# Performance work log

Hardware: AMD Instinct MI355X
Metric: run time of the kernel (lower is better)

The kernel has to match this reference:

```python
import jax, jax.numpy as jnp
import numpy as np

B = 8192
D = 64      # core_size = size ** (1/nr_cores), size = 4096, nr_cores = 2
R = 4       # TT rank
SIZE = D * D


def setup_inputs() -> dict:
    key = jax.random.key(0)
    k_x, k_c0, k_c1, k_b = jax.random.split(key, 4)
    core_std = (2.0 / D) ** 0.5  # kaiming_normal on (-1, d, d) blocks
    x = jax.random.normal(k_x, (B, SIZE), dtype=jnp.float32)
    core0 = core_std * jax.random.normal(k_c0, (D, D, D, R, 1), dtype=jnp.float32)
    core1 = core_std * jax.random.normal(k_c1, (D, D, D, 1, R), dtype=jnp.float32)
    bound = (6.0 / SIZE) ** 0.5  # kaiming_uniform on (1, out_dim)
    bias = jax.random.uniform(k_b, (SIZE,), dtype=jnp.float32, minval=-bound, maxval=bound)
    return {"x": x, "core0": core0, "core1": core1, "bias": bias}


def reference(x, core0, core1, bias):
    # BTT.forward with nr_cores=2, d=D, rank=R
    b = x.shape[0]
    # idx=0: t=1 -> j=D, i=1 ; z: (B, j=D, x=D, i=1, a=1), core: (j=D, x=D, y=D, i=1, b=R, a=1)
    z = x.reshape(b, D, D, 1, 1)
    c0 = core0.reshape(D, D, D, 1, R, 1)
    z = jnp.einsum('Bjxia,jxyiba->Bjyib', z, c0)  # (B, D, D, 1, R)
    # idx=1: t=0 -> j=1, i=D ; z: (B, 1, D, D, R), core: (1, D, D, D, 1, R)
    z = z.reshape(b, 1, D, D, R)
    c1 = core1.reshape(1, D, D, D, 1, R)
    z = jnp.einsum('Bjxia,jxyiba->Bjyib', z, c1)  # (B, 1, D, D, 1)
    return z.reshape(b, -1) + bias
```

## Files before the change

### kernel.cpp

```cpp
#include <hip/hip_runtime.h>


typedef unsigned short ushort_t;
typedef __attribute__((ext_vector_type(8))) short sfrag8;
typedef __attribute__((ext_vector_type(4))) float f32x4;

__device__ inline ushort_t f2bf(float f) {
    unsigned int u = __builtin_bit_cast(unsigned int, f);
    u += 0x7fffu + ((u >> 16) & 1u);
    return (ushort_t)(u >> 16);
}

__global__ __launch_bounds__(256) void prep_c0t(const float* __restrict__ c0,
                                                ushort_t* __restrict__ c0t) {
    __shared__ float tile[64][65];
    const int t = threadIdx.x;
    const int ub = blockIdx.x * 64;
    const int cb = blockIdx.y * 64;
#pragma unroll
    for (int it = 0; it < 16; ++it) {
        const int r = it * 4 + (t >> 6);
        const int c = t & 63;
        tile[r][c] = c0[(size_t)(ub + r) * 256 + cb + c];
    }
    __syncthreads();
#pragma unroll
    for (int it = 0; it < 16; ++it) {
        const int r = it * 4 + (t >> 6);
        const int c = t & 63;
        c0t[(size_t)(cb + r) * 4096 + ub + c] = f2bf(tile[c][r]);
    }
}

__global__ __launch_bounds__(256) void prep_c1t(const float* __restrict__ c1,
                                                ushort_t* __restrict__ c1t) {
    const int y  = blockIdx.x;
    const int jg = blockIdx.y;
    const int t  = threadIdx.x;
#pragma unroll
    for (int iter = 0; iter < 2; ++iter) {
        const int idx = iter * 256 + t;
        const int jj  = idx >> 6;
        const int i   = idx & 63;
        const int j   = jg * 8 + jj;
        const float4 v = *(const float4*)(c1 + (size_t)(j * 64 + y) * 256 + i * 4);
        const ushort4 pk = make_ushort4(f2bf(v.x), f2bf(v.y), f2bf(v.z), f2bf(v.w));
        *(ushort4*)(c1t + ((size_t)y * 64 + i) * 256 + j * 4) = pk;
    }
}

__global__ __launch_bounds__(512, 4) void btt_main(
    const float* __restrict__ x,
    const ushort_t* __restrict__ c0t,
    const ushort_t* __restrict__ c1t,
    const float* __restrict__ bias,
    float* __restrict__ out)
{
    __shared__ __align__(16) char z1[32 * 512];

    const int t    = threadIdx.x;
    const int w    = t >> 6;
    const int lane = t & 63;
    const int quad = lane >> 4;
    const int l16  = lane & 15;

    const int i0 = blockIdx.x * 8;
    const int b0 = blockIdx.y * 32;

    const int mb = w >> 2;
    const int yq = w & 3;
    const int y  = yq * 16 + l16;

    f32x4 acc[8];
#pragma unroll
    for (int ii = 0; ii < 8; ++ii) {
        const float bv = bias[y * 64 + i0 + ii];
        acc[ii] = (f32x4){bv, bv, bv, bv};
    }

    const ushort_t* aptr = c0t + (size_t)(i0 * 4 + l16) * 4096 + quad * 8;
    const float*    xptr = x   + (size_t)(b0 + l16) * 4096 + quad * 8;
    const ushort_t* bzp  = c1t + ((size_t)y * 64 + i0) * 256 + quad * 8;

#pragma unroll 1
    for (int g = 0; g < 8; ++g) {
        const int jc = (g * 8 + w) * 64;

        sfrag8 A[2][2];
#pragma unroll
        for (int nt = 0; nt < 2; ++nt)
#pragma unroll
            for (int kh = 0; kh < 2; ++kh)
                A[nt][kh] = *(const sfrag8*)(aptr + (size_t)nt * 16 * 4096 + jc + kh * 32);

        sfrag8 Bf[2][2];
#pragma unroll
        for (int bt = 0; bt < 2; ++bt)
#pragma unroll
            for (int kh = 0; kh < 2; ++kh) {
                const float* p = xptr + (size_t)bt * 16 * 4096 + jc + kh * 32;
                const float4 v0 = *(const float4*)p;
                const float4 v1 = *(const float4*)(p + 4);
                sfrag8 pk;
                pk[0] = (short)f2bf(v0.x); pk[1] = (short)f2bf(v0.y);
                pk[2] = (short)f2bf(v0.z); pk[3] = (short)f2bf(v0.w);
                pk[4] = (short)f2bf(v1.x); pk[5] = (short)f2bf(v1.y);
                pk[6] = (short)f2bf(v1.z); pk[7] = (short)f2bf(v1.w);
                Bf[bt][kh] = pk;
            }

        sfrag8 bz[8];
#pragma unroll
        for (int ii = 0; ii < 8; ++ii)
            bz[ii] = *(const sfrag8*)(bzp + ii * 256 + g * 32);

#pragma unroll
        for (int nt = 0; nt < 2; ++nt)
#pragma unroll
            for (int bt = 0; bt < 2; ++bt) {
                f32x4 d = {0.f, 0.f, 0.f, 0.f};
                d = __builtin_amdgcn_mfma_f32_16x16x32_bf16(A[nt][0], Bf[bt][0], d, 0, 0, 0);
                d = __builtin_amdgcn_mfma_f32_16x16x32_bf16(A[nt][1], Bf[bt][1], d, 0, 0, 0);
                const int bb = bt * 16 + l16;
                const int ii = nt * 4 + quad;
                const ushort4 pk = make_ushort4(f2bf(d[0]), f2bf(d[1]),
                                                f2bf(d[2]), f2bf(d[3]));
                *(ushort4*)(z1 + bb * 512 + ((ii * 64 + w * 8) ^ ((bb & 7) << 4))) = pk;
            }

        __syncthreads();

        const int ar = mb * 16 + l16;
        const int as = (ar & 7) << 4;
#pragma unroll
        for (int ii = 0; ii < 8; ++ii) {
            const sfrag8 az = *(const sfrag8*)(z1 + ar * 512
                                               + ((ii * 64 + quad * 16) ^ as));
            acc[ii] = __builtin_amdgcn_mfma_f32_16x16x32_bf16(az, bz[ii], acc[ii], 0, 0, 0);
        }

        __syncthreads();
    }

#pragma unroll
    for (int reg = 0; reg < 4; ++reg) {
        const int bb = mb * 16 + quad * 4 + reg;
        float* dst = out + (size_t)(b0 + bb) * 4096 + y * 64 + i0;
        *(float4*)dst       = make_float4(acc[0][reg], acc[1][reg],
                                          acc[2][reg], acc[3][reg]);
        *(float4*)(dst + 4) = make_float4(acc[4][reg], acc[5][reg],
                                          acc[6][reg], acc[7][reg]);
    }
}

extern "C" void kernel_launch(void* const* d_in, const int* in_sizes, int n_in,
                              void* d_out, int out_size, void* d_ws, size_t ws_size,
                              hipStream_t stream) {
    const float* x     = (const float*)d_in[0];
    const float* core0 = (const float*)d_in[1];
    const float* core1 = (const float*)d_in[2];
    const float* bias  = (const float*)d_in[3];
    float* out = (float*)d_out;

    ushort_t* c0t = (ushort_t*)d_ws;
    ushort_t* c1t = (ushort_t*)d_ws + (size_t)256 * 4096;

    prep_c0t<<<dim3(64, 4), 256, 0, stream>>>(core0, c0t);
    prep_c1t<<<dim3(64, 8), 256, 0, stream>>>(core1, c1t);

    dim3 grid(64 / 8, 8192 / 32);
    btt_main<<<grid, 512, 0, stream>>>(x, c0t, c1t, bias, out);
}
```

Baseline: 520.0 us.

## Stage x through LDS with coalesced register prefetch and XCD-aware block mapping

Each wave now loads x rows with fully coalesced float4 reads, prefetches the next j-chunk into registers, converts to bf16 and stores into a swizzled LDS tile from which MFMA B fragments are read. The old per-lane strided global reads of x are removed. The grid is flattened and remapped so that blocks on the same XCD share batch rows, improving L2 locality. A barrier macro with an explicit lgkmcnt wait is added. The cost is 32KB more LDS per block, which may reduce occupancy, plus an extra barrier per iteration.

```diff
diff --git a/kernel.cpp b/kernel.cpp
--- a/kernel.cpp
+++ b/kernel.cpp
@@ -10,6 +10,12 @@
     u += 0x7fffu + ((u >> 16) & 1u);
     return (ushort_t)(u >> 16);
 }
+
+#define BARRIER() do {                                     \
+    asm volatile("s_waitcnt lgkmcnt(0)" ::: "memory");     \
+    __builtin_amdgcn_s_barrier();                          \
+    asm volatile("" ::: "memory");                         \
+} while (0)
 
 __global__ __launch_bounds__(256) void prep_c0t(const float* __restrict__ c0,
                                                 ushort_t* __restrict__ c0t) {
@@ -56,6 +62,7 @@
     const float* __restrict__ bias,
     float* __restrict__ out)
 {
+    __shared__ __align__(16) char xlds[32 * 1024];
     __shared__ __align__(16) char z1[32 * 512];
 
     const int t    = threadIdx.x;
@@ -64,8 +71,11 @@
     const int quad = lane >> 4;
     const int l16  = lane & 15;
 
-    const int i0 = blockIdx.x * 8;
-    const int b0 = blockIdx.y * 32;
+    const int bid = blockIdx.x;
+    const int xcd = bid & 7;
+    const int idx = bid >> 3;
+    const int b0  = xcd * 1024 + (idx >> 3) * 32;
+    const int i0  = (idx & 7) * 8;
 
     const int mb = w >> 2;
     const int yq = w & 3;
@@ -79,13 +89,31 @@
     }
 
     const ushort_t* aptr = c0t + (size_t)(i0 * 4 + l16) * 4096 + quad * 8;
-    const float*    xptr = x   + (size_t)(b0 + l16) * 4096 + quad * 8;
     const ushort_t* bzp  = c1t + ((size_t)y * 64 + i0) * 256 + quad * 8;
+    const float* xsrc = x + (size_t)(b0 + w) * 4096 + lane * 4;
+
+    float4 xr[8];
+#pragma unroll
+    for (int c = 0; c < 4; ++c)
+#pragma unroll
+        for (int h = 0; h < 2; ++h)
+            xr[c * 2 + h] = *(const float4*)(xsrc + (size_t)c * 8 * 4096 + h * 256);
 
 #pragma unroll 1
     for (int g = 0; g < 8; ++g) {
         const int jc = (g * 8 + w) * 64;
 
+#pragma unroll
+        for (int c = 0; c < 4; ++c)
+#pragma unroll
+            for (int h = 0; h < 2; ++h) {
+                const float4 v = xr[c * 2 + h];
+                const ushort4 pk = make_ushort4(f2bf(v.x), f2bf(v.y),
+                                                f2bf(v.z), f2bf(v.w));
+                *(ushort4*)(xlds + (c * 8 + w) * 1024
+                            + ((h * 512 + lane * 8) ^ (w << 4))) = pk;
+            }
+
         sfrag8 A[2][2];
 #pragma unroll
         for (int nt = 0; nt < 2; ++nt)
@@ -93,53 +121,60 @@
             for (int kh = 0; kh < 2; ++kh)
                 A[nt][kh] = *(const sfrag8*)(aptr + (size_t)nt * 16 * 4096 + jc + kh * 32);
 
-        sfrag8 Bf[2][2];
-#pragma unroll
-        for (int bt = 0; bt < 2; ++bt)
-#pragma unroll
-            for (int kh = 0; kh < 2; ++kh) {
-                const float* p = xptr + (size_t)bt * 16 * 4096 + jc + kh * 32;
-                const float4 v0 = *(const float4*)p;
-                const float4 v1 = *(const float4*)(p + 4);
-                sfrag8 pk;
-                pk[0] = (short)f2bf(v0.x); pk[1] = (short)f2bf(v0.y);
-                pk[2] = (short)f2bf(v0.z); pk[3] = (short)f2bf(v0.w);
-                pk[4] = (short)f2bf(v1.x); pk[5] = (short)f2bf(v1.y);
-                pk[6] = (short)f2bf(v1.z); pk[7] = (short)f2bf(v1.w);
-                Bf[bt][kh] = pk;
-            }
+        if (g != 7) {
+#pragma unroll
+            for (int c = 0; c < 4; ++c)
+#pragma unroll
+                for (int h = 0; h < 2; ++h)
+                    xr[c * 2 + h] = *(const float4*)(xsrc + (size_t)c * 8 * 4096
+                                                     + (g + 1) * 512 + h * 256);
+        }
+
+        BARRIER();
+
+        {
+            sfrag8 Bf[2][2];
+#pragma unroll
+            for (int bt = 0; bt < 2; ++bt)
+#pragma unroll
+                for (int kh = 0; kh < 2; ++kh)
+                    Bf[bt][kh] = *(const sfrag8*)(xlds + (bt * 16 + l16) * 1024
+                                  + ((w * 128 + kh * 64 + quad * 16) ^ ((l16 & 7) << 4)));
+
+#pragma unroll
+            for (int nt = 0; nt < 2; ++nt)
+#pragma unroll
+                for (int bt = 0; bt < 2; ++bt) {
+                    f32x4 d = {0.f, 0.f, 0.f, 0.f};
+                    d = __builtin_amdgcn_mfma_f32_16x16x32_bf16(A[nt][0], Bf[bt][0], d, 0, 0, 0);
+                    d = __builtin_amdgcn_mfma_f32_16x16x32_bf16(A[nt][1], Bf[bt][1], d, 0, 0, 0);
+                    const int bb = bt * 16 + l16;
+                    const int ii = nt * 4 + quad;
+                    const ushort4 pk = make_ushort4(f2bf(d[0]), f2bf(d[1]),
+                                                    f2bf(d[2]), f2bf(d[3]));
+                    *(ushort4*)(z1 + bb * 512 + ((ii * 64 + w * 8) ^ ((bb & 7) << 4))) = pk;
+                }
+        }
 
         sfrag8 bz[8];
 #pragma unroll
         for (int ii = 0; ii < 8; ++ii)
             bz[ii] = *(const sfrag8*)(bzp + ii * 256 + g * 32);
 
-#pragma unroll
-        for (int nt = 0; nt < 2; ++nt)
-#pragma unroll
-            for (int bt = 0; bt < 2; ++bt) {
-                f32x4 d = {0.f, 0.f, 0.f, 0.f};
-                d = __builtin_amdgcn_mfma_f32_16x16x32_bf16(A[nt][0], Bf[bt][0], d, 0, 0, 0);
-                d = __builtin_amdgcn_mfma_f32_16x16x32_bf16(A[nt][1], Bf[bt][1], d, 0, 0, 0);
-                const int bb = bt * 16 + l16;
-                const int ii = nt * 4 + quad;
-                const ushort4 pk = make_ushort4(f2bf(d[0]), f2bf(d[1]),
-                                                f2bf(d[2]), f2bf(d[3]));
-                *(ushort4*)(z1 + bb * 512 + ((ii * 64 + w * 8) ^ ((bb & 7) << 4))) = pk;
+        BARRIER();
+
+        {
+            const int ar = mb * 16 + l16;
+            const int as = (ar & 7) << 4;
+#pragma unroll
+            for (int ii = 0; ii < 8; ++ii) {
+                const sfrag8 az = *(const sfrag8*)(z1 + ar * 512
+                                                   + ((ii * 64 + quad * 16) ^ as));
+                acc[ii] = __builtin_amdgcn_mfma_f32_16x16x32_bf16(az, bz[ii], acc[ii], 0, 0, 0);
             }
-
-        __syncthreads();
-
-        const int ar = mb * 16 + l16;
-        const int as = (ar & 7) << 4;
-#pragma unroll
-        for (int ii = 0; ii < 8; ++ii) {
-            const sfrag8 az = *(const sfrag8*)(z1 + ar * 512
-                                               + ((ii * 64 + quad * 16) ^ as));
-            acc[ii] = __builtin_amdgcn_mfma_f32_16x16x32_bf16(az, bz[ii], acc[ii], 0, 0, 0);
         }
 
-        __syncthreads();
+        BARRIER();
     }
 
 #pragma unroll
@@ -168,6 +203,5 @@
     prep_c0t<<<dim3(64, 4), 256, 0, stream>>>(core0, c0t);
     prep_c1t<<<dim3(64, 8), 256, 0, stream>>>(core1, c1t);
 
-    dim3 grid(64 / 8, 8192 / 32);
-    btt_main<<<grid, 512, 0, stream>>>(x, c0t, c1t, bias, out);
-}
+    btt_main<<<dim3(2048), 512, 0, stream>>>(x, c0t, c1t, bias, out);
+}
```

Result: faster. 461.3 us (-11.3%).
